# Performance work log

Hardware: AMD Instinct MI355X
Metric: run time of the kernel (lower is better)

Reference implementation:

```python
import jax, jax.numpy as jnp
import numpy as np

N, C, S, NS = 65536, 64, 8, 16  # points, channels, share_planes, nsample
CS = C // S
EPS = 1e-5


def _bn(x, g, b, m, v):
    # BatchNorm1d in eval mode over the last (channel) axis
    return (x - m) * (g * jax.lax.rsqrt(v + EPS)) + b


def setup_inputs() -> dict:
    key = jax.random.key(0)
    ks = jax.random.split(key, 32)
    rn = lambda k, s: jax.random.normal(k, s, jnp.float32)
    un = lambda k, s: jax.random.uniform(k, s, jnp.float32, 0.5, 1.5)
    return {
        "p": rn(ks[0], (N, 3)),
        "x": rn(ks[1], (N, C)),
        "idx": jax.random.randint(ks[2], (N, NS), 0, N),
        "Wq": rn(ks[3], (C, C)) * 0.1, "bq": rn(ks[4], (C,)) * 0.1,
        "Wk": rn(ks[5], (C, C)) * 0.1, "bk": rn(ks[6], (C,)) * 0.1,
        "Wv": rn(ks[7], (C, C)) * 0.1, "bv": rn(ks[8], (C,)) * 0.1,
        "Wp1": rn(ks[9], (3, 3)) * 0.3, "bp1": rn(ks[10], (3,)) * 0.1,
        "pg": un(ks[11], (3,)), "pb": rn(ks[12], (3,)) * 0.1,
        "pm": rn(ks[13], (3,)) * 0.1, "pv": un(ks[14], (3,)),
        "Wp2": rn(ks[15], (C, 3)) * 0.3, "bp2": rn(ks[16], (C,)) * 0.1,
        "wg1": un(ks[17], (C,)), "wb1": rn(ks[18], (C,)) * 0.1,
        "wm1": rn(ks[19], (C,)) * 0.1, "wv1": un(ks[20], (C,)),
        "Ww1": rn(ks[21], (CS, C)) * 0.1, "bw1": rn(ks[22], (CS,)) * 0.1,
        "wg2": un(ks[23], (CS,)), "wb2": rn(ks[24], (CS,)) * 0.1,
        "wm2": rn(ks[25], (CS,)) * 0.1, "wv2": un(ks[26], (CS,)),
        "Ww2": rn(ks[27], (CS, CS)) * 0.1, "bw2": rn(ks[28], (CS,)) * 0.1,
    }


def _forward(p, x, idx, Wq, bq, Wk, bk, Wv, bv, Wp1, bp1, pg, pb, pm, pv,
             Wp2, bp2, wg1, wb1, wm1, wv1, Ww1, bw1, wg2, wb2, wm2, wv2, Ww2, bw2):
    xq = x @ Wq.T + bq                      # [N, C]
    xk = (x @ Wk.T + bk)[idx]               # [N, NS, C] neighbor gather
    xv = (x @ Wv.T + bv)[idx]               # [N, NS, C]
    pr = p[idx] - p[:, None, :]             # [N, NS, 3] relative coords (queryandgroup use_xyz)
    # linear_p: Conv1d(3,3,1) -> BN(3) -> ReLU -> Conv1d(3,C,1) (pointwise)
    t = jax.nn.relu(_bn(pr @ Wp1.T + bp1, pg, pb, pm, pv))
    pr = t @ Wp2.T + bp2                    # [N, NS, C] positional encoding
    # out_planes // mid_planes == 1, so p_r.view(...).sum(2) is identity
    w = xk - xq[:, None, :] + pr            # [N, NS, C] relation
    # linear_w: BN(C) -> ReLU -> Conv(C,C/S) -> BN(C/S) -> ReLU -> Conv(C/S,C/S)
    w = jax.nn.relu(_bn(w, wg1, wb1, wm1, wv1))
    w = jax.nn.relu(_bn(w @ Ww1.T + bw1, wg2, wb2, wm2, wv2))
    w = w @ Ww2.T + bw2                     # [N, NS, C//S]
    w = jax.nn.softmax(w, axis=1)           # softmax over the neighbor axis
    out = ((xv + pr).reshape(N, NS, S, CS) * w[:, :, None, :]).sum(axis=1)
    return out.reshape(N, C)


def reference(p, x, idx, Wq, bq, Wk, bk, Wv, bv, Wp1, bp1, pg, pb, pm, pv,
              Wp2, bp2, wg1, wb1, wm1, wv1, Ww1, bw1, wg2, wb2, wm2, wv2, Ww2, bw2):
    return _forward(p, x, idx, Wq, bq, Wk, bk, Wv, bv, Wp1, bp1, pg, pb, pm, pv,
                    Wp2, bp2, wg1, wb1, wm1, wv1, Ww1, bw1, wg2, wb2, wm2, wv2, Ww2, bw2)
```

## Files before the change

kernel.cpp:

```cpp
#include <hip/hip_runtime.h>

#define NPTS 65536
#define EPSV 1e-5f

typedef unsigned int uint_t;
typedef unsigned short ushort_t;
typedef __attribute__((ext_vector_type(8))) short short8;
typedef __attribute__((ext_vector_type(4))) float float4v;

__device__ __forceinline__ ushort_t f2bf(float f) {
    unsigned u = __float_as_uint(f);
    unsigned r = (u + 0x7fffu + ((u >> 16) & 1u)) >> 16;
    return (ushort_t)r;
}

__device__ __forceinline__ float rdlane(float v, int j) {
    return __uint_as_float(__builtin_amdgcn_readlane(__float_as_uint(v), j));
}

__global__ __launch_bounds__(256) void k_qkv(
    const float* __restrict__ x,
    const float* __restrict__ Wq, const float* __restrict__ bq,
    const float* __restrict__ Wk, const float* __restrict__ bk,
    const float* __restrict__ Wv, const float* __restrict__ bv,
    float* __restrict__ xq, uint_t* __restrict__ kvp)
{
    __shared__ __align__(16) ushort_t sA[64 * 72];
    __shared__ __align__(16) ushort_t sB[192 * 72];

    const int tid  = threadIdx.x;
    const int lane = tid & 63;
    const int w    = tid >> 6;
    const int n0   = blockIdx.x * 64;

    const float4* xg = (const float4*)(x + (size_t)n0 * 64);
#pragma unroll
    for (int i = 0; i < 4; ++i) {
        int f = i * 256 + tid;
        float4 v = xg[f];
        int r = f >> 4, c4 = f & 15;
        uint2 pk;
        pk.x = (uint_t)f2bf(v.x) | ((uint_t)f2bf(v.y) << 16);
        pk.y = (uint_t)f2bf(v.z) | ((uint_t)f2bf(v.w) << 16);
        *(uint2*)(sA + r * 72 + c4 * 4) = pk;
    }
#pragma unroll
    for (int i = 0; i < 12; ++i) {
        const float* src = (i < 4) ? Wq : (i < 8) ? Wk : Wv;
        int f = i * 256 + tid;
        int r = f >> 4, c4 = f & 15;
        float4 v = ((const float4*)src)[(i & 3) * 256 + tid];
        uint2 pk;
        pk.x = (uint_t)f2bf(v.x) | ((uint_t)f2bf(v.y) << 16);
        pk.y = (uint_t)f2bf(v.z) | ((uint_t)f2bf(v.w) << 16);
        *(uint2*)(sB + r * 72 + c4 * 4) = pk;
    }
    __syncthreads();

    const int quad = lane >> 4;
    const int cn   = lane & 15;
    const int mrow = (w << 4) + cn;

    short8 a0 = *(const short8*)(sA + mrow * 72 + quad * 8);
    short8 a1 = *(const short8*)(sA + mrow * 72 + 32 + quad * 8);

    float4v acc[12];
#pragma unroll
    for (int t = 0; t < 12; ++t) {
        const int brow = t * 16 + cn;
        short8 b0 = *(const short8*)(sB + brow * 72 + quad * 8);
        short8 b1 = *(const short8*)(sB + brow * 72 + 32 + quad * 8);
        float4v c = {0.f, 0.f, 0.f, 0.f};
        c = __builtin_amdgcn_mfma_f32_16x16x32_bf16(a0, b0, c, 0, 0, 0);
        c = __builtin_amdgcn_mfma_f32_16x16x32_bf16(a1, b1, c, 0, 0, 0);
        acc[t] = c;
    }

    const int orow = n0 + (w << 4) + quad * 4;
#pragma unroll
    for (int t = 0; t < 4; ++t) {
        int o = t * 16 + cn;
        float bqv = bq[o], bkv = bk[o], bvv = bv[o];
        float4v aq = acc[t], ak = acc[4 + t], av = acc[8 + t];
#pragma unroll
        for (int r = 0; r < 4; ++r) {
            size_t base = (size_t)(orow + r) * 64 + o;
            xq[base]  = aq[r] + bqv;
            kvp[base] = (uint_t)f2bf(ak[r] + bkv) | ((uint_t)f2bf(av[r] + bvv) << 16);
        }
    }
}

__global__ __launch_bounds__(256, 4) void k_attn(
    const float* __restrict__ p, const int* __restrict__ idx,
    const float* __restrict__ xq, const uint_t* __restrict__ kvp,
    const float* __restrict__ Wp1, const float* __restrict__ bp1,
    const float* __restrict__ pg, const float* __restrict__ pb,
    const float* __restrict__ pm, const float* __restrict__ pv,
    const float* __restrict__ Wp2, const float* __restrict__ bp2,
    const float* __restrict__ wg1, const float* __restrict__ wb1,
    const float* __restrict__ wm1, const float* __restrict__ wv1,
    const float* __restrict__ Ww1, const float* __restrict__ bw1,
    const float* __restrict__ wg2, const float* __restrict__ wb2,
    const float* __restrict__ wm2, const float* __restrict__ wv2,
    const float* __restrict__ Ww2, const float* __restrict__ bw2,
    float* __restrict__ out)
{
    __shared__ float sw[4][16 * 68];
    __shared__ float sh[4][16 * 9];
    __shared__ float sW1[8 * 68];

    const int tid   = threadIdx.x;
    const int wid   = __builtin_amdgcn_readfirstlane(tid >> 6);
    const int lane  = tid & 63;
    const int nbase = blockIdx.x * 16 + wid * 4;

#pragma unroll
    for (int e = tid; e < 544; e += 256) {
        int r = e / 68, c = e - r * 68;
        sW1[e] = (c < 64) ? Ww1[r * 64 + c] : 0.f;
    }
    __syncthreads();

    float* wrel = sw[wid];
    float* hb   = sh[wid];

    const int* idxr = idx + (size_t)nbase * 16;

    uint_t ga[16], gb[16];
    auto issueF = [&](int pt, uint_t (&dst)[16]) {
#pragma unroll
        for (int j = 0; j < 16; ++j) {
            int id = __builtin_amdgcn_readfirstlane(idxr[pt * 16 + j]);
            dst[j] = kvp[(size_t)id * 64 + lane];
        }
    };

    issueF(0, ga);
    issueF(1, gb);

    int   idv[4];
    float xqc[4];
#pragma unroll
    for (int pt = 0; pt < 4; ++pt) {
        idv[pt] = idxr[pt * 16 + (lane & 15)];
        xqc[pt] = xq[(size_t)(nbase + pt) * 64 + lane];
    }
    float gpx[4], gpy[4], gpz[4];
#pragma unroll
    for (int pt = 0; pt < 4; ++pt) {
        gpx[pt] = p[idv[pt] * 3 + 0];
        gpy[pt] = p[idv[pt] * 3 + 1];
        gpz[pt] = p[idv[pt] * 3 + 2];
    }

    float w100 = Wp1[0], w101 = Wp1[1], w102 = Wp1[2];
    float w110 = Wp1[3], w111 = Wp1[4], w112 = Wp1[5];
    float w120 = Wp1[6], w121 = Wp1[7], w122 = Wp1[8];
    float sp0 = pg[0] * rsqrtf(pv[0] + EPSV);
    float sp1 = pg[1] * rsqrtf(pv[1] + EPSV);
    float sp2 = pg[2] * rsqrtf(pv[2] + EPSV);
    float off0 = (bp1[0] - pm[0]) * sp0 + pb[0];
    float off1 = (bp1[1] - pm[1]) * sp1 + pb[1];
    float off2 = (bp1[2] - pm[2]) * sp2 + pb[2];

    float s1 = wg1[lane] * rsqrtf(wv1[lane] + EPSV);
    float o1 = wb1[lane] - wm1[lane] * s1;
    float wp2x = Wp2[lane * 3 + 0], wp2y = Wp2[lane * 3 + 1], wp2z = Wp2[lane * 3 + 2];
    float peb = bp2[lane];

    const int m  = lane & 7;
    const int j0 = lane >> 3;
    float s2 = wg2[m] * rsqrtf(wv2[m] + EPSV);
    float o2 = wb2[m] - wm2[m] * s2;
    float bw1v = bw1[m];
    float bw2v = bw2[m];
    float w2r[8];
#pragma unroll
    for (int mm = 0; mm < 8; ++mm) w2r[mm] = Ww2[m * 8 + mm];

    float t0a[4], t1a[4], t2a[4];
#pragma unroll
    for (int pt = 0; pt < 4; ++pt) {
        int n = nbase + pt;
        float pcx = p[n * 3 + 0], pcy = p[n * 3 + 1], pcz = p[n * 3 + 2];
        float prx = gpx[pt] - pcx, pry = gpy[pt] - pcy, prz = gpz[pt] - pcz;
        t0a[pt] = fmaxf(fmaf(fmaf(prx, w100, fmaf(pry, w101, prz * w102)), sp0, off0), 0.f);
        t1a[pt] = fmaxf(fmaf(fmaf(prx, w110, fmaf(pry, w111, prz * w112)), sp1, off1), 0.f);
        t2a[pt] = fmaxf(fmaf(fmaf(prx, w120, fmaf(pry, w121, prz * w122)), sp2, off2), 0.f);
    }

    auto computeF = [&](int pt, uint_t (&g)[16]) {
        float t0v = t0a[pt], t1v = t1a[pt], t2v = t2a[pt];
        float xqv = xqc[pt];
        float vpe[16];
#pragma unroll
        for (int j = 0; j < 16; ++j) {
            float tt0 = rdlane(t0v, j);
            float tt1 = rdlane(t1v, j);
            float tt2 = rdlane(t2v, j);
            float pe = fmaf(tt0, wp2x, fmaf(tt1, wp2y, fmaf(tt2, wp2z, peb)));
            float xkj = __uint_as_float(g[j] << 16);
            float xvj = __uint_as_float(g[j] & 0xffff0000u);
            vpe[j] = xvj + pe;
            wrel[j * 68 + lane] = fmaxf(fmaf(xkj - xqv + pe, s1, o1), 0.f);
        }
        asm volatile("s_waitcnt lgkmcnt(0)" ::: "memory");
        __builtin_amdgcn_wave_barrier();

#pragma unroll
        for (int pi = 0; pi < 2; ++pi) {
            int j = j0 + pi * 8;
            float acc = bw1v;
            const float* wr = wrel + j * 68;
#pragma unroll
            for (int c4 = 0; c4 < 16; ++c4) {
                float4 u = *((const float4*)(sW1 + m * 68 + c4 * 4));
                const float* r = wr + c4 * 4;
                acc = fmaf(r[0], u.x, fmaf(r[1], u.y, fmaf(r[2], u.z, fmaf(r[3], u.w, acc))));
            }
            hb[j * 9 + m] = fmaxf(fmaf(acc, s2, o2), 0.f);
        }
        asm volatile("s_waitcnt lgkmcnt(0)" ::: "memory");
        __builtin_amdgcn_wave_barrier();

#pragma unroll
        for (int pi = 0; pi < 2; ++pi) {
            int j = j0 + pi * 8;
            float acc = bw2v;
#pragma unroll
            for (int mm = 0; mm < 8; ++mm) acc = fmaf(hb[j * 9 + mm], w2r[mm], acc);
            asm volatile("s_waitcnt lgkmcnt(0)" ::: "memory");
            __builtin_amdgcn_wave_barrier();
            hb[j * 9 + m] = acc;
        }
        asm volatile("s_waitcnt lgkmcnt(0)" ::: "memory");
        __builtin_amdgcn_wave_barrier();

        float mx = -1e30f;
        float e[16];
#pragma unroll
        for (int j = 0; j < 16; ++j) { e[j] = hb[j * 9 + m]; mx = fmaxf(mx, e[j]); }
        float ssum = 0.f;
#pragma unroll
        for (int j = 0; j < 16; ++j) { e[j] = __expf(e[j] - mx); ssum += e[j]; }
        float inv = 1.f / ssum;
        float acc = 0.f;
#pragma unroll
        for (int j = 0; j < 16; ++j) acc = fmaf(vpe[j], e[j], acc);
        asm volatile("s_waitcnt lgkmcnt(0)" ::: "memory");
        __builtin_amdgcn_wave_barrier();
        out[(size_t)(nbase + pt) * 64 + lane] = acc * inv;
    };

    computeF(0, ga);
    issueF(2, ga);
    computeF(1, gb);
    issueF(3, gb);
    computeF(2, ga);
    computeF(3, gb);
}

extern "C" void kernel_launch(void* const* d_in, const int* in_sizes, int n_in,
                              void* d_out, int out_size, void* d_ws, size_t ws_size,
                              hipStream_t stream) {
    const float* p   = (const float*)d_in[0];
    const float* x   = (const float*)d_in[1];
    const int*   idx = (const int*)d_in[2];
    const float* Wq  = (const float*)d_in[3];  const float* bq  = (const float*)d_in[4];
    const float* Wk  = (const float*)d_in[5];  const float* bk  = (const float*)d_in[6];
    const float* Wv  = (const float*)d_in[7];  const float* bv  = (const float*)d_in[8];
    const float* Wp1 = (const float*)d_in[9];  const float* bp1 = (const float*)d_in[10];
    const float* pg  = (const float*)d_in[11]; const float* pb  = (const float*)d_in[12];
    const float* pm  = (const float*)d_in[13]; const float* pv  = (const float*)d_in[14];
    const float* Wp2 = (const float*)d_in[15]; const float* bp2 = (const float*)d_in[16];
    const float* wg1 = (const float*)d_in[17]; const float* wb1 = (const float*)d_in[18];
    const float* wm1 = (const float*)d_in[19]; const float* wv1 = (const float*)d_in[20];
    const float* Ww1 = (const float*)d_in[21]; const float* bw1 = (const float*)d_in[22];
    const float* wg2 = (const float*)d_in[23]; const float* wb2 = (const float*)d_in[24];
    const float* wm2 = (const float*)d_in[25]; const float* wv2 = (const float*)d_in[26];
    const float* Ww2 = (const float*)d_in[27]; const float* bw2 = (const float*)d_in[28];

    float*  xqw = (float*)d_ws;
    uint_t* kvw = (uint_t*)((char*)d_ws + (size_t)NPTS * 64 * sizeof(float));
    float*  outp = (float*)d_out;

    k_qkv<<<dim3(NPTS / 64), dim3(256), 0, stream>>>(x, Wq, bq, Wk, bk, Wv, bv, xqw, kvw);
    k_attn<<<dim3(NPTS / 16), dim3(256), 0, stream>>>(p, idx, xqw, kvw,
                                                      Wp1, bp1, pg, pb, pm, pv, Wp2, bp2,
                                                      wg1, wb1, wm1, wv1, Ww1, bw1,
                                                      wg2, wb2, wm2, wv2, Ww2, bw2, outp);
}
```

Measured before the change: 211.4 us.

## Use bf16 MFMA for linear_w matmuls and shuffle-based softmax in attention kernel

Replaces the scalar FMA loops for the two small linear_w projections (64->8 and 8->8) with 16x16x32 bf16 MFMA instructions. Weights are packed into registers instead of shared memory, and relation rows are converted to bf16 on the fly. The softmax over neighbors now reduces with lane shuffles and writes normalized weights to LDS. Occupancy hint drops from 4 to 3 blocks, and the bf16 rounding of intermediate activations may reduce accuracy.

```diff
diff --git a/kernel.cpp b/kernel.cpp
--- a/kernel.cpp
+++ b/kernel.cpp
@@ -8,15 +8,40 @@
 typedef __attribute__((ext_vector_type(8))) short short8;
 typedef __attribute__((ext_vector_type(4))) float float4v;
 
+union U8 { uint4 u; short8 s; };
+
 __device__ __forceinline__ ushort_t f2bf(float f) {
     unsigned u = __float_as_uint(f);
     unsigned r = (u + 0x7fffu + ((u >> 16) & 1u)) >> 16;
     return (ushort_t)r;
 }
 
-__device__ __forceinline__ float rdlane(float v, int j) {
-    return __uint_as_float(__builtin_amdgcn_readlane(__float_as_uint(v), j));
-}
+__device__ __forceinline__ uint_t pkrn(uint_t lo, uint_t hi) {
+    return ((lo + 0x8000u) >> 16) | ((hi + 0x8000u) & 0xffff0000u);
+}
+
+__device__ __forceinline__ short8 packA(const float* p8) {
+    uint4 a = *(const uint4*)p8;
+    uint4 b = *(const uint4*)(p8 + 4);
+    U8 c;
+    c.u.x = pkrn(a.x, a.y); c.u.y = pkrn(a.z, a.w);
+    c.u.z = pkrn(b.x, b.y); c.u.w = pkrn(b.z, b.w);
+    return c.s;
+}
+
+__device__ __forceinline__ short8 packG(const float* p8) {
+    float4 a = *(const float4*)p8;
+    float4 b = *(const float4*)(p8 + 4);
+    U8 c;
+    c.u.x = pkrn(__float_as_uint(a.x), __float_as_uint(a.y));
+    c.u.y = pkrn(__float_as_uint(a.z), __float_as_uint(a.w));
+    c.u.z = pkrn(__float_as_uint(b.x), __float_as_uint(b.y));
+    c.u.w = pkrn(__float_as_uint(b.z), __float_as_uint(b.w));
+    return c.s;
+}
+
+#define WBAR() do { asm volatile("s_waitcnt lgkmcnt(0)" ::: "memory"); \
+                    __builtin_amdgcn_wave_barrier(); } while (0)
 
 __global__ __launch_bounds__(256) void k_qkv(
     const float* __restrict__ x,
@@ -91,7 +116,7 @@
     }
 }
 
-__global__ __launch_bounds__(256, 4) void k_attn(
+__global__ __launch_bounds__(256, 3) void k_attn(
     const float* __restrict__ p, const int* __restrict__ idx,
     const float* __restrict__ xq, const uint_t* __restrict__ kvp,
     const float* __restrict__ Wp1, const float* __restrict__ bp1,
@@ -106,24 +131,24 @@
     const float* __restrict__ Ww2, const float* __restrict__ bw2,
     float* __restrict__ out)
 {
-    __shared__ float sw[4][16 * 68];
-    __shared__ float sh[4][16 * 9];
-    __shared__ float sW1[8 * 68];
+    __shared__ __align__(16) float sw[4][16 * 68];
+    __shared__ __align__(16) float shl[4][16 * 36];
+    __shared__ float swg[4][16 * 9 + 4];
 
     const int tid   = threadIdx.x;
     const int wid   = __builtin_amdgcn_readfirstlane(tid >> 6);
     const int lane  = tid & 63;
     const int nbase = blockIdx.x * 16 + wid * 4;
 
-#pragma unroll
-    for (int e = tid; e < 544; e += 256) {
-        int r = e / 68, c = e - r * 68;
-        sW1[e] = (c < 64) ? Ww1[r * 64 + c] : 0.f;
-    }
-    __syncthreads();
-
     float* wrel = sw[wid];
-    float* hb   = sh[wid];
+    float* hL   = shl[wid];
+    float* wgt  = swg[wid];
+
+    const int cm  = lane & 15;
+    const int q   = lane >> 4;
+    const int m8  = lane & 7;
+    const int cmc = cm & 7;
+    const bool colv = cm < 8;
 
     const int* idxr = idx + (size_t)nbase * 16;
 
@@ -139,11 +164,13 @@
     issueF(0, ga);
     issueF(1, gb);
 
+    for (int i = lane; i < 16 * 36; i += 64) hL[i] = 0.f;
+
     int   idv[4];
     float xqc[4];
 #pragma unroll
     for (int pt = 0; pt < 4; ++pt) {
-        idv[pt] = idxr[pt * 16 + (lane & 15)];
+        idv[pt] = idxr[pt * 16 + cm];
         xqc[pt] = xq[(size_t)(nbase + pt) * 64 + lane];
     }
     float gpx[4], gpy[4], gpz[4];
@@ -169,15 +196,21 @@
     float wp2x = Wp2[lane * 3 + 0], wp2y = Wp2[lane * 3 + 1], wp2z = Wp2[lane * 3 + 2];
     float peb = bp2[lane];
 
-    const int m  = lane & 7;
-    const int j0 = lane >> 3;
-    float s2 = wg2[m] * rsqrtf(wv2[m] + EPSV);
-    float o2 = wb2[m] - wm2[m] * s2;
-    float bw1v = bw1[m];
-    float bw2v = bw2[m];
-    float w2r[8];
-#pragma unroll
-    for (int mm = 0; mm < 8; ++mm) w2r[mm] = Ww2[m * 8 + mm];
+    float s2c = wg2[cmc] * rsqrtf(wv2[cmc] + EPSV);
+    float o2c = wb2[cmc] - wm2[cmc] * s2c;
+    float bw1c = bw1[cmc];
+
+    short8 bf1a, bf1b, bf2;
+    {
+        const float* r1 = Ww1 + cmc * 64 + q * 8;
+        short8 t1a = packG(r1);
+        short8 t1b = packG(r1 + 32);
+        short8 t2  = packG(Ww2 + cmc * 8);
+        U8 z; z.u = make_uint4(0u, 0u, 0u, 0u);
+        bf1a = colv ? t1a : z.s;
+        bf1b = colv ? t1b : z.s;
+        bf2  = (colv && q == 0) ? t2 : z.s;
+    }
 
     float t0a[4], t1a[4], t2a[4];
 #pragma unroll
@@ -196,61 +229,55 @@
         float vpe[16];
 #pragma unroll
         for (int j = 0; j < 16; ++j) {
-            float tt0 = rdlane(t0v, j);
-            float tt1 = rdlane(t1v, j);
-            float tt2 = rdlane(t2v, j);
+            float tt0 = __uint_as_float(__builtin_amdgcn_readlane(__float_as_uint(t0v), j));
+            float tt1 = __uint_as_float(__builtin_amdgcn_readlane(__float_as_uint(t1v), j));
+            float tt2 = __uint_as_float(__builtin_amdgcn_readlane(__float_as_uint(t2v), j));
             float pe = fmaf(tt0, wp2x, fmaf(tt1, wp2y, fmaf(tt2, wp2z, peb)));
             float xkj = __uint_as_float(g[j] << 16);
             float xvj = __uint_as_float(g[j] & 0xffff0000u);
             vpe[j] = xvj + pe;
             wrel[j * 68 + lane] = fmaxf(fmaf(xkj - xqv + pe, s1, o1), 0.f);
         }
-        asm volatile("s_waitcnt lgkmcnt(0)" ::: "memory");
-        __builtin_amdgcn_wave_barrier();
-
-#pragma unroll
-        for (int pi = 0; pi < 2; ++pi) {
-            int j = j0 + pi * 8;
-            float acc = bw1v;
-            const float* wr = wrel + j * 68;
-#pragma unroll
-            for (int c4 = 0; c4 < 16; ++c4) {
-                float4 u = *((const float4*)(sW1 + m * 68 + c4 * 4));
-                const float* r = wr + c4 * 4;
-                acc = fmaf(r[0], u.x, fmaf(r[1], u.y, fmaf(r[2], u.z, fmaf(r[3], u.w, acc))));
-            }
-            hb[j * 9 + m] = fmaxf(fmaf(acc, s2, o2), 0.f);
-        }
-        asm volatile("s_waitcnt lgkmcnt(0)" ::: "memory");
-        __builtin_amdgcn_wave_barrier();
-
-#pragma unroll
-        for (int pi = 0; pi < 2; ++pi) {
-            int j = j0 + pi * 8;
-            float acc = bw2v;
-#pragma unroll
-            for (int mm = 0; mm < 8; ++mm) acc = fmaf(hb[j * 9 + mm], w2r[mm], acc);
-            asm volatile("s_waitcnt lgkmcnt(0)" ::: "memory");
-            __builtin_amdgcn_wave_barrier();
-            hb[j * 9 + m] = acc;
-        }
-        asm volatile("s_waitcnt lgkmcnt(0)" ::: "memory");
-        __builtin_amdgcn_wave_barrier();
-
-        float mx = -1e30f;
-        float e[16];
-#pragma unroll
-        for (int j = 0; j < 16; ++j) { e[j] = hb[j * 9 + m]; mx = fmaxf(mx, e[j]); }
-        float ssum = 0.f;
-#pragma unroll
-        for (int j = 0; j < 16; ++j) { e[j] = __expf(e[j] - mx); ssum += e[j]; }
-        float inv = 1.f / ssum;
+        WBAR();
+
+        short8 a1a = packA(wrel + cm * 68 + q * 8);
+        short8 a1b = packA(wrel + cm * 68 + 32 + q * 8);
+        float4v d1 = {0.f, 0.f, 0.f, 0.f};
+        d1 = __builtin_amdgcn_mfma_f32_16x16x32_bf16(a1a, bf1a, d1, 0, 0, 0);
+        d1 = __builtin_amdgcn_mfma_f32_16x16x32_bf16(a1b, bf1b, d1, 0, 0, 0);
+#pragma unroll
+        for (int r = 0; r < 4; ++r) {
+            float hv = fmaxf(fmaf(d1[r] + bw1c, s2c, o2c), 0.f);
+            if (colv) hL[(q * 4 + r) * 36 + cm] = hv;
+        }
+        WBAR();
+
+        short8 a2 = packA(hL + cm * 36 + q * 8);
+        float4v d2 = {0.f, 0.f, 0.f, 0.f};
+        d2 = __builtin_amdgcn_mfma_f32_16x16x32_bf16(a2, bf2, d2, 0, 0, 0);
+
+        float mx = fmaxf(fmaxf(d2[0], d2[1]), fmaxf(d2[2], d2[3]));
+        mx = fmaxf(mx, __shfl_xor(mx, 16));
+        mx = fmaxf(mx, __shfl_xor(mx, 32));
+        float e0 = __expf(d2[0] - mx), e1 = __expf(d2[1] - mx);
+        float e2 = __expf(d2[2] - mx), e3 = __expf(d2[3] - mx);
+        float ss = e0 + e1 + e2 + e3;
+        ss += __shfl_xor(ss, 16);
+        ss += __shfl_xor(ss, 32);
+        float inv = 1.f / ss;
+        if (colv) {
+            wgt[(q * 4 + 0) * 9 + cm] = e0 * inv;
+            wgt[(q * 4 + 1) * 9 + cm] = e1 * inv;
+            wgt[(q * 4 + 2) * 9 + cm] = e2 * inv;
+            wgt[(q * 4 + 3) * 9 + cm] = e3 * inv;
+        }
+        WBAR();
+
         float acc = 0.f;
 #pragma unroll
-        for (int j = 0; j < 16; ++j) acc = fmaf(vpe[j], e[j], acc);
-        asm volatile("s_waitcnt lgkmcnt(0)" ::: "memory");
-        __builtin_amdgcn_wave_barrier();
-        out[(size_t)(nbase + pt) * 64 + lane] = acc * inv;
+        for (int j = 0; j < 16; ++j) acc = fmaf(wgt[j * 9 + m8], vpe[j], acc);
+        WBAR();
+        out[(size_t)(nbase + pt) * 64 + lane] = acc;
     };
 
     computeF(0, ga);
```

Result: faster. 190.4 us (-9.9%).
